# Performance work log

Measured on AMD Instinct MI355X. Metric: run time of the kernel, lower is better.

The kernel has to match this reference:

```python
import jax, jax.numpy as jnp
import numpy as np

D_MODEL = 1024
NUM_HEADS = 16
D_HEAD = D_MODEL // NUM_HEADS
MAX_LEN = 16384
BATCH = 4
SEQ = 1024


def setup_inputs() -> dict:
    key = jax.random.key(0)
    ks = jax.random.split(key, 10)
    s = 1.0 / np.sqrt(D_MODEL)
    return {
        "q_in": jax.random.normal(ks[0], (BATCH, SEQ, D_MODEL), jnp.float32),
        "k_in": jax.random.normal(ks[1], (BATCH, SEQ, D_MODEL), jnp.float32),
        "v_in": jax.random.normal(ks[2], (BATCH, SEQ, D_MODEL), jnp.float32),
        "Wq": jax.random.normal(ks[3], (D_MODEL, D_MODEL), jnp.float32) * s,
        "bq": jnp.zeros((D_MODEL,), jnp.float32),
        "Wk": jax.random.normal(ks[4], (D_MODEL, D_MODEL), jnp.float32) * s,
        "bk": jnp.zeros((D_MODEL,), jnp.float32),
        "Wv": jax.random.normal(ks[5], (D_MODEL, D_MODEL), jnp.float32) * s,
        "bv": jnp.zeros((D_MODEL,), jnp.float32),
        "Er": jax.random.normal(ks[6], (MAX_LEN, D_HEAD), jnp.float32),
    }


def _skew(QEr):
    # QEr: [B, H, S, S] -> pad one zero column on the left, reshape, drop row 0
    B, H, S, _ = QEr.shape
    padded = jnp.pad(QEr, ((0, 0), (0, 0), (0, 0), (1, 0)))  # [B,H,S,S+1]
    reshaped = padded.reshape(B, H, S + 1, S)
    return reshaped[:, :, 1:, :]  # [B,H,S,S]


def reference(q_in, k_in, v_in, Wq, bq, Wk, bk, Wv, bv, Er):
    B, S, _ = q_in.shape
    H, Dh = NUM_HEADS, D_HEAD
    # projections, split into heads: [B, H, S, Dh]
    q = (q_in @ Wq + bq).reshape(B, S, H, Dh).transpose(0, 2, 1, 3)
    k = (k_in @ Wk + bk).reshape(B, S, H, Dh).transpose(0, 2, 1, 3)
    v = (v_in @ Wv + bv).reshape(B, S, H, Dh).transpose(0, 2, 1, 3)
    # relative position scores: Er slice [S, Dh]
    Er_sl = Er[MAX_LEN - S:, :]
    QEr = jnp.einsum('bhsd,td->bhst', q, Er_sl)  # [B,H,S,S]
    Srel = _skew(QEr)
    QK = jnp.einsum('bhsd,bhtd->bhst', q, k)
    attn = (QK + Srel) / jnp.sqrt(jnp.asarray(Dh, q.dtype))
    attn = jax.nn.softmax(attn, axis=-1)
    out = jnp.einsum('bhst,bhtd->bhsd', attn, v)  # [B,H,S,Dh]
    out = out.transpose(0, 2, 1, 3).reshape(B, S, H * Dh)
    return out
```

## Files before the change

kernel.cpp:

```cpp
#include <hip/hip_runtime.h>
#include <hip/hip_bf16.h>
#include <cstdint>

#define S_LEN 1024
#define DMODEL 1024
#define NHEADS 16
#define DHEAD 64
#define MAXLEN 16384
#define BATCH 4

typedef __attribute__((ext_vector_type(8))) short bf16x8;
typedef __attribute__((ext_vector_type(4))) float f32x4;

#define AS1(p) ((const __attribute__((address_space(1))) unsigned int*)(p))
#define AS3(p) ((__attribute__((address_space(3))) unsigned int*)(p))

__device__ inline unsigned short f2b(float f) {
  unsigned int u = __float_as_uint(f);
  unsigned int r = (u + 0x7FFFu + ((u >> 16) & 1u)) >> 16;
  return (unsigned short)r;
}
__device__ inline float b2f(unsigned short u) {
  return __uint_as_float(((unsigned int)u) << 16);
}

#define LDSWZ(row, slot) (((row) << 6) + (((slot) ^ ((row) & 7)) << 3))

__global__ __launch_bounds__(256) void wt_er_convert(
    const float* __restrict__ W0, const float* __restrict__ W1, const float* __restrict__ W2,
    unsigned short* __restrict__ T0, unsigned short* __restrict__ T1, unsigned short* __restrict__ T2,
    const float* __restrict__ Er, unsigned short* __restrict__ Erb) {
  const int z = blockIdx.z;
  if (z == 3) {
    const int o = blockIdx.y * 32 + blockIdx.x;
    if (o < 64) {
      const int i = o * 1024 + threadIdx.x * 4;
      float4 f = *(const float4*)(Er + (size_t)(MAXLEN - S_LEN) * DHEAD + i);
      Erb[i] = f2b(f.x); Erb[i + 1] = f2b(f.y);
      Erb[i + 2] = f2b(f.z); Erb[i + 3] = f2b(f.w);
    }
    return;
  }
  const float* W = (z == 0) ? W0 : (z == 1) ? W1 : W2;
  unsigned short* WT = (z == 0) ? T0 : (z == 1) ? T1 : T2;
  __shared__ float t[32][33];
  const int bi = blockIdx.y * 32, bj = blockIdx.x * 32;
  const int r = threadIdx.x >> 3, c4 = (threadIdx.x & 7) * 4;
  float4 f = *(const float4*)&W[(size_t)(bi + r) * DMODEL + bj + c4];
  t[r][c4] = f.x; t[r][c4 + 1] = f.y; t[r][c4 + 2] = f.z; t[r][c4 + 3] = f.w;
  __syncthreads();
  ushort4 u;
  u.x = f2b(t[c4][r]); u.y = f2b(t[c4 + 1][r]);
  u.z = f2b(t[c4 + 2][r]); u.w = f2b(t[c4 + 3][r]);
  *(ushort4*)&WT[(size_t)(bj + r) * DMODEL + bi + c4] = u;
}

__global__ __launch_bounds__(256) void xconvert3(
    const float* __restrict__ X0, const float* __restrict__ X1, const float* __restrict__ X2,
    unsigned short* __restrict__ B0, unsigned short* __restrict__ B1, unsigned short* __restrict__ B2) {
  const int z = blockIdx.z;
  const float* X = (z == 0) ? X0 : (z == 1) ? X1 : X2;
  unsigned short* B = (z == 0) ? B0 : (z == 1) ? B1 : B2;
  size_t i = ((size_t)blockIdx.x * 256 + threadIdx.x) * 16;
  union { unsigned short h[16]; int4 v[2]; } u;
#pragma unroll
  for (int r = 0; r < 4; ++r) {
    float4 f = *(const float4*)(X + i + r * 4);
    u.h[r * 4 + 0] = f2b(f.x); u.h[r * 4 + 1] = f2b(f.y);
    u.h[r * 4 + 2] = f2b(f.z); u.h[r * 4 + 3] = f2b(f.w);
  }
  *(int4*)(B + i) = u.v[0];
  *(int4*)(B + i + 8) = u.v[1];
}

__global__ __launch_bounds__(256) void proj_glds3(
    const unsigned short* __restrict__ Xq, const unsigned short* __restrict__ Xk,
    const unsigned short* __restrict__ Xv,
    const unsigned short* __restrict__ T0, const unsigned short* __restrict__ T1,
    const unsigned short* __restrict__ T2,
    const float* __restrict__ b0, const float* __restrict__ b1, const float* __restrict__ b2,
    unsigned short* __restrict__ O0, unsigned short* __restrict__ O1,
    unsigned short* __restrict__ O2) {
  const int z = blockIdx.z;
  const unsigned short* X = (z == 0) ? Xq : (z == 1) ? Xk : Xv;
  const unsigned short* WT = (z == 0) ? T0 : (z == 1) ? T1 : T2;
  const float* bias = (z == 0) ? b0 : (z == 1) ? b1 : b2;
  unsigned short* Out = (z == 0) ? O0 : (z == 1) ? O1 : O2;
  const float osc = (z == 0) ? 0.125f : 1.0f;
  __shared__ unsigned short As[128 * 64];
  __shared__ unsigned short Bs[128 * 64];
  const int tid = threadIdx.x;
  const int l = tid & 63, w = tid >> 6;
  const int o = blockIdx.y * 8 + blockIdx.x;
  const int lid = (o & 7) * 32 + (o >> 3);
  const int bm = (lid >> 3) * 128, bn = (lid & 7) * 128;
  const int wr = (w >> 1) * 64, wc = (w & 1) * 64;
  const int lrow = l >> 3;
  const int slotlog = (l & 7) ^ (lrow & 7);
  const unsigned short* Xa = X + (size_t)(bm + lrow) * DMODEL + slotlog * 8;
  const unsigned short* Wa = WT + (size_t)(bn + lrow) * DMODEL + slotlog * 8;
  f32x4 acc[4][4] = {};
  for (int k0 = 0; k0 < DMODEL; k0 += 64) {
    __syncthreads();
#pragma unroll
    for (int j = 0; j < 4; ++j) {
      int r8 = (w * 4 + j) * 8;
      __builtin_amdgcn_global_load_lds(AS1(Xa + (size_t)r8 * DMODEL + k0),
                                       AS3(&As[(w * 4 + j) * 512]), 16, 0, 0);
      __builtin_amdgcn_global_load_lds(AS1(Wa + (size_t)r8 * DMODEL + k0),
                                       AS3(&Bs[(w * 4 + j) * 512]), 16, 0, 0);
    }
    __syncthreads();
#pragma unroll
    for (int ks = 0; ks < 2; ++ks) {
      bf16x8 a[4], b[4];
#pragma unroll
      for (int f = 0; f < 4; ++f) {
        int row = wr + f * 16 + (l & 15);
        a[f] = *(const bf16x8*)&As[LDSWZ(row, ks * 4 + (l >> 4))];
        int col = wc + f * 16 + (l & 15);
        b[f] = *(const bf16x8*)&Bs[LDSWZ(col, ks * 4 + (l >> 4))];
      }
#pragma unroll
      for (int i = 0; i < 4; ++i)
#pragma unroll
        for (int j = 0; j < 4; ++j)
          acc[i][j] = __builtin_amdgcn_mfma_f32_16x16x32_bf16(a[i], b[j], acc[i][j], 0, 0, 0);
    }
  }
#pragma unroll
  for (int i = 0; i < 4; ++i) {
    int m = bm + wr + i * 16 + ((l >> 4) << 2);
#pragma unroll
    for (int j = 0; j < 4; ++j) {
      int n = bn + wc + j * 16 + (l & 15);
      float bv = bias[n];
#pragma unroll
      for (int e = 0; e < 4; ++e)
        Out[(size_t)(m + e) * DMODEL + n] = f2b((acc[i][j][e] + bv) * osc);
    }
  }
}

__global__ __launch_bounds__(256) void qer_mfma(const unsigned short* __restrict__ qp,
    const unsigned short* __restrict__ Erb, unsigned short* __restrict__ G, int bh0) {
  const int bh = bh0 + blockIdx.z;
  const int b = bh >> 4, h = bh & 15;
  __shared__ unsigned short As[128 * 64];
  __shared__ unsigned short Bs[128 * 64];
  const int tid = threadIdx.x, l = tid & 63, wid = tid >> 6;
  const int bm = blockIdx.y * 128, bn = blockIdx.x * 128;
  const int wr = (wid >> 1) * 64, wc = (wid & 1) * 64;
  const unsigned short* qb = qp + (size_t)b * S_LEN * DMODEL + h * DHEAD;
  unsigned short* Gc = G + (size_t)blockIdx.z * S_LEN * S_LEN;
#pragma unroll
  for (int r = 0; r < 4; ++r) {
    int s = r * 256 + tid;
    int row = s >> 3, sl = s & 7;
    *(int4*)&As[LDSWZ(row, sl)] = *(const int4*)(qb + (size_t)(bm + row) * DMODEL + sl * 8);
    *(int4*)&Bs[LDSWZ(row, sl)] = *(const int4*)(Erb + (size_t)(bn + row) * DHEAD + sl * 8);
  }
  if (blockIdx.x == 0 && tid < 128) {
    int s = bm + tid;
    if (s < S_LEN - 1) Gc[(size_t)s * S_LEN + s + 1] = 0;
  }
  __syncthreads();
  f32x4 acc[4][4] = {};
#pragma unroll
  for (int ks = 0; ks < 2; ++ks) {
    bf16x8 a[4], b[4];
#pragma unroll
    for (int f = 0; f < 4; ++f) {
      int row = wr + f * 16 + (l & 15);
      a[f] = *(const bf16x8*)&As[LDSWZ(row, ks * 4 + (l >> 4))];
      int col = wc + f * 16 + (l & 15);
      b[f] = *(const bf16x8*)&Bs[LDSWZ(col, ks * 4 + (l >> 4))];
    }
#pragma unroll
    for (int i = 0; i < 4; ++i)
#pragma unroll
      for (int j = 0; j < 4; ++j)
        acc[i][j] = __builtin_amdgcn_mfma_f32_16x16x32_bf16(a[i], b[j], acc[i][j], 0, 0, 0);
  }
#pragma unroll
  for (int i = 0; i < 4; ++i) {
    int m = bm + wr + i * 16 + ((l >> 4) << 2);
#pragma unroll
    for (int j = 0; j < 4; ++j) {
      int n = bn + wc + j * 16 + (l & 15);
#pragma unroll
      for (int e = 0; e < 4; ++e) {
        int s = m + e;
        int hi = (n >= 1023 - s);
        int r_ = hi ? s : s - 1;
        int t_ = hi ? (n + s - 1023) : (n + s + 1);
        if (r_ >= 0)
          Gc[(size_t)r_ * S_LEN + t_] = f2b(acc[i][j][e]);
      }
    }
  }
}

__global__ __launch_bounds__(256) void attn_skew(const unsigned short* __restrict__ qp,
    const unsigned short* __restrict__ kp, const unsigned short* __restrict__ vp,
    const unsigned short* __restrict__ G, float* __restrict__ out, int bh0) {
  const int bh = bh0 + blockIdx.y;
  const int b = bh >> 4, h = bh & 15;
  const int s0 = blockIdx.x * 64;
  __shared__ unsigned short Qs[64 * 64];
  __shared__ unsigned short Ks[64 * 64];
  __shared__ unsigned short Vt[64 * 64];
  __shared__ unsigned short Ps[4][16 * 64];
  const int tid = threadIdx.x, l = tid & 63, w = tid >> 6;
  const int lg = l >> 4, li = l & 15;
  const unsigned short* qb = qp + (size_t)b * S_LEN * DMODEL + h * DHEAD;
  const unsigned short* kb = kp + (size_t)b * S_LEN * DMODEL + h * DHEAD;
  const unsigned short* vb = vp + (size_t)b * S_LEN * DMODEL + h * DHEAD;
  const unsigned short* Gb = G + (size_t)blockIdx.y * S_LEN * S_LEN;

#pragma unroll
  for (int r = 0; r < 2; ++r) {
    int s = r * 256 + tid;
    int row = s >> 3, sl = s & 7;
    *(int4*)&Qs[LDSWZ(row, sl)] = *(const int4*)(qb + (size_t)(s0 + row) * DMODEL + sl * 8);
  }
  __syncthreads();
  bf16x8 qf[2];
#pragma unroll
  for (int ks = 0; ks < 2; ++ks)
    qf[ks] = *(const bf16x8*)&Qs[LDSWZ(w * 16 + li, ks * 4 + lg)];

  const int lrow = l >> 3;
  const int chk = (l & 7) ^ lrow;
  const unsigned short* Ka = kb + (size_t)(w * 8 + lrow) * DMODEL + chk * 8;

  f32x4 o4[4] = {};
  float lsum[4] = {0.f, 0.f, 0.f, 0.f};
  int sg[4];
  const unsigned short* gp[4];
#pragma unroll
  for (int i = 0; i < 4; ++i) {
    sg[i] = s0 + w * 16 + (lg << 2) + i;
    gp[i] = Gb + (size_t)sg[i] * S_LEN + li;
  }
  const int pr = tid & 31, dh0 = (tid >> 5) * 8;
  const float L2E = 1.44269504f;
  const float SHF = 16.f * 1.44269504f;

  for (int ti = 0; ti < 16; ++ti) {
    const int t0 = ti * 64;
    __syncthreads();
    __builtin_amdgcn_global_load_lds(AS1(Ka + (size_t)t0 * DMODEL),
                                     AS3(&Ks[(w * 64) * 8]), 16, 0, 0);
    __builtin_amdgcn_global_load_lds(AS1(Ka + (size_t)(t0 + 32) * DMODEL),
                                     AS3(&Ks[(256 + w * 64) * 8]), 16, 0, 0);
    {
      const unsigned short* v0p = vb + (size_t)(t0 + pr * 2) * DMODEL + dh0;
      union { int4 v; unsigned short hh[8]; } va, vc;
      va.v = *(const int4*)v0p;
      vc.v = *(const int4*)(v0p + DMODEL);
      unsigned int* vtw = (unsigned int*)Vt;
#pragma unroll
      for (int j = 0; j < 8; ++j) {
        int dh = dh0 + j;
        int widx = dh * 32 + (((pr >> 2) ^ (dh & 7)) << 2) + (pr & 3);
        vtw[widx] = (unsigned int)va.hh[j] | ((unsigned int)vc.hh[j] << 16);
      }
    }
    __syncthreads();
    unsigned short rv[4][4];
#pragma unroll
    for (int f = 0; f < 4; ++f)
#pragma unroll
      for (int i = 0; i < 4; ++i)
        rv[f][i] = gp[i][t0 + f * 16];
    f32x4 sa[4] = {};
#pragma unroll
    for (int ks = 0; ks < 2; ++ks)
#pragma unroll
      for (int f = 0; f < 4; ++f) {
        bf16x8 kf = *(const bf16x8*)&Ks[LDSWZ(f * 16 + li, ks * 4 + lg)];
        sa[f] = __builtin_amdgcn_mfma_f32_16x16x32_bf16(qf[ks], kf, sa[f], 0, 0, 0);
      }
    unsigned short* Pw = &Ps[w][0];
#pragma unroll
    for (int f = 0; f < 4; ++f) {
#pragma unroll
      for (int i = 0; i < 4; ++i) {
        float sv = sa[f][i] + b2f(rv[f][i]);
        float pv = __builtin_exp2f(__builtin_fmaf(sv, L2E, -SHF));
        unsigned int pu = __float_as_uint(pv) & 0xffff0000u;
        lsum[i] += __uint_as_float(pu);
        int prow = (lg << 2) + i, pcol = f * 16 + li;
        Pw[LDSWZ(prow, pcol >> 3) + (pcol & 7)] = (unsigned short)(pu >> 16);
      }
    }
#pragma unroll
    for (int ks = 0; ks < 2; ++ks) {
      bf16x8 pf = *(const bf16x8*)&Pw[LDSWZ(li, ks * 4 + lg)];
#pragma unroll
      for (int f = 0; f < 4; ++f) {
        bf16x8 vf = *(const bf16x8*)&Vt[LDSWZ(f * 16 + li, ks * 4 + lg)];
        o4[f] = __builtin_amdgcn_mfma_f32_16x16x32_bf16(pf, vf, o4[f], 0, 0, 0);
      }
    }
  }
#pragma unroll
  for (int off = 8; off >= 1; off >>= 1)
#pragma unroll
    for (int i = 0; i < 4; ++i) lsum[i] += __shfl_xor(lsum[i], off);
#pragma unroll
  for (int i = 0; i < 4; ++i) {
    float inv = 1.f / lsum[i];
#pragma unroll
    for (int f = 0; f < 4; ++f)
      out[(size_t)(b * S_LEN + sg[i]) * DMODEL + h * DHEAD + f * 16 + li] = o4[f][i] * inv;
  }
}

extern "C" void kernel_launch(void* const* d_in, const int* in_sizes, int n_in,
                              void* d_out, int out_size, void* d_ws, size_t ws_size,
                              hipStream_t stream) {
  (void)in_sizes; (void)n_in; (void)out_size;
  const float* q_in = (const float*)d_in[0];
  const float* k_in = (const float*)d_in[1];
  const float* v_in = (const float*)d_in[2];
  const float* Wq   = (const float*)d_in[3];
  const float* bq   = (const float*)d_in[4];
  const float* Wk   = (const float*)d_in[5];
  const float* bk   = (const float*)d_in[6];
  const float* Wv   = (const float*)d_in[7];
  const float* bv   = (const float*)d_in[8];
  const float* Er   = (const float*)d_in[9];
  float* out = (float*)d_out;

  char* ws = (char*)d_ws;
  const size_t MB = (size_t)1 << 20;
  unsigned short* wtq = (unsigned short*)(ws);
  unsigned short* wtk = (unsigned short*)(ws + 2 * MB);
  unsigned short* wtv = (unsigned short*)(ws + 4 * MB);
  unsigned short* erb = (unsigned short*)(ws + 6 * MB);
  unsigned short* qp  = (unsigned short*)(ws + 8 * MB);
  unsigned short* kp  = (unsigned short*)(ws + 16 * MB);
  unsigned short* vp  = (unsigned short*)(ws + 24 * MB);
  unsigned short* xq  = (unsigned short*)(ws + 32 * MB);
  unsigned short* xk  = (unsigned short*)(ws + 40 * MB);
  unsigned short* xv  = (unsigned short*)(ws + 48 * MB);
  unsigned short* G   = (unsigned short*)(ws + 56 * MB);

  const size_t gavail = (ws_size > 56 * MB) ? (ws_size - 56 * MB) : 0;
  int chunk = (int)(gavail / (2 * MB));
  if (chunk < 1) chunk = 1;
  if (chunk > 64) chunk = 64;

  dim3 blk(256);
  hipLaunchKernelGGL(wt_er_convert, dim3(32, 32, 4), blk, 0, stream,
                     Wq, Wk, Wv, wtq, wtk, wtv, Er, erb);
  hipLaunchKernelGGL(xconvert3, dim3(1024, 1, 3), blk, 0, stream,
                     q_in, k_in, v_in, xq, xk, xv);

  dim3 gproj(DMODEL / 128, (BATCH * S_LEN) / 128, 3);
  hipLaunchKernelGGL(proj_glds3, gproj, blk, 0, stream,
                     xq, xk, xv, wtq, wtk, wtv, bq, bk, bv, qp, kp, vp);

  for (int bh0 = 0; bh0 < BATCH * NHEADS; bh0 += chunk) {
    int nb = BATCH * NHEADS - bh0;
    if (nb > chunk) nb = chunk;
    dim3 gqer(S_LEN / 128, S_LEN / 128, nb);
    hipLaunchKernelGGL(qer_mfma, gqer, blk, 0, stream, qp, erb, G, bh0);
    dim3 gattn(S_LEN / 64, nb);
    hipLaunchKernelGGL(attn_skew, gattn, blk, 0, stream, qp, kp, vp, G, out, bh0);
  }
}
```

Baseline: 161.8 us.

## Merge convert kernels, prefetch skew tile, remap attention blocks, seed MFMA accumulator

Folds the weight/Er and activation fp32-to-bf16 conversions into a single launch to save one kernel launch. In the attention kernel, the next tile's skewed relative-position values are prefetched into registers (double-buffered A/B) while the current tile computes, hiding global load latency. The relative term is now used as the initial MFMA accumulator instead of being added afterwards. Block indices are also remapped so consecutive blocks go to different heads, which may change L2 and XCD locality; the cost is higher register pressure and an unrolled body.

```diff
diff --git a/kernel.cpp b/kernel.cpp
--- a/kernel.cpp
+++ b/kernel.cpp
@@ -26,11 +26,28 @@
 
 #define LDSWZ(row, slot) (((row) << 6) + (((slot) ^ ((row) & 7)) << 3))
 
-__global__ __launch_bounds__(256) void wt_er_convert(
+__global__ __launch_bounds__(256) void convert_all(
     const float* __restrict__ W0, const float* __restrict__ W1, const float* __restrict__ W2,
     unsigned short* __restrict__ T0, unsigned short* __restrict__ T1, unsigned short* __restrict__ T2,
-    const float* __restrict__ Er, unsigned short* __restrict__ Erb) {
+    const float* __restrict__ Er, unsigned short* __restrict__ Erb,
+    const float* __restrict__ X0, const float* __restrict__ X1, const float* __restrict__ X2,
+    unsigned short* __restrict__ B0, unsigned short* __restrict__ B1, unsigned short* __restrict__ B2) {
   const int z = blockIdx.z;
+  if (z >= 4) {
+    const float* X = (z == 4) ? X0 : (z == 5) ? X1 : X2;
+    unsigned short* B = (z == 4) ? B0 : (z == 5) ? B1 : B2;
+    size_t i = (((size_t)blockIdx.y * 32 + blockIdx.x) * 256 + threadIdx.x) * 16;
+    union { unsigned short hh[16]; int4 v[2]; } u;
+#pragma unroll
+    for (int r = 0; r < 4; ++r) {
+      float4 f = *(const float4*)(X + i + r * 4);
+      u.hh[r * 4 + 0] = f2b(f.x); u.hh[r * 4 + 1] = f2b(f.y);
+      u.hh[r * 4 + 2] = f2b(f.z); u.hh[r * 4 + 3] = f2b(f.w);
+    }
+    *(int4*)(B + i) = u.v[0];
+    *(int4*)(B + i + 8) = u.v[1];
+    return;
+  }
   if (z == 3) {
     const int o = blockIdx.y * 32 + blockIdx.x;
     if (o < 64) {
@@ -53,24 +70,6 @@
   u.x = f2b(t[c4][r]); u.y = f2b(t[c4 + 1][r]);
   u.z = f2b(t[c4 + 2][r]); u.w = f2b(t[c4 + 3][r]);
   *(ushort4*)&WT[(size_t)(bj + r) * DMODEL + bi + c4] = u;
-}
-
-__global__ __launch_bounds__(256) void xconvert3(
-    const float* __restrict__ X0, const float* __restrict__ X1, const float* __restrict__ X2,
-    unsigned short* __restrict__ B0, unsigned short* __restrict__ B1, unsigned short* __restrict__ B2) {
-  const int z = blockIdx.z;
-  const float* X = (z == 0) ? X0 : (z == 1) ? X1 : X2;
-  unsigned short* B = (z == 0) ? B0 : (z == 1) ? B1 : B2;
-  size_t i = ((size_t)blockIdx.x * 256 + threadIdx.x) * 16;
-  union { unsigned short h[16]; int4 v[2]; } u;
-#pragma unroll
-  for (int r = 0; r < 4; ++r) {
-    float4 f = *(const float4*)(X + i + r * 4);
-    u.h[r * 4 + 0] = f2b(f.x); u.h[r * 4 + 1] = f2b(f.y);
-    u.h[r * 4 + 2] = f2b(f.z); u.h[r * 4 + 3] = f2b(f.w);
-  }
-  *(int4*)(B + i) = u.v[0];
-  *(int4*)(B + i + 8) = u.v[1];
 }
 
 __global__ __launch_bounds__(256) void proj_glds3(
@@ -203,10 +202,14 @@
 
 __global__ __launch_bounds__(256) void attn_skew(const unsigned short* __restrict__ qp,
     const unsigned short* __restrict__ kp, const unsigned short* __restrict__ vp,
-    const unsigned short* __restrict__ G, float* __restrict__ out, int bh0) {
-  const int bh = bh0 + blockIdx.y;
+    const unsigned short* __restrict__ G, float* __restrict__ out, int bh0, int nb) {
+  const int o = blockIdx.y * 16 + blockIdx.x;
+  const int q8 = nb * 2;
+  const int lid = (o & 7) * q8 + (o >> 3);
+  const int s0 = (lid & 15) * 64;
+  const int bhl = lid >> 4;
+  const int bh = bh0 + bhl;
   const int b = bh >> 4, h = bh & 15;
-  const int s0 = blockIdx.x * 64;
   __shared__ unsigned short Qs[64 * 64];
   __shared__ unsigned short Ks[64 * 64];
   __shared__ unsigned short Vt[64 * 64];
@@ -216,7 +219,7 @@
   const unsigned short* qb = qp + (size_t)b * S_LEN * DMODEL + h * DHEAD;
   const unsigned short* kb = kp + (size_t)b * S_LEN * DMODEL + h * DHEAD;
   const unsigned short* vb = vp + (size_t)b * S_LEN * DMODEL + h * DHEAD;
-  const unsigned short* Gb = G + (size_t)blockIdx.y * S_LEN * S_LEN;
+  const unsigned short* Gb = G + (size_t)bhl * S_LEN * S_LEN;
 
 #pragma unroll
   for (int r = 0; r < 2; ++r) {
@@ -224,6 +227,18 @@
     int row = s >> 3, sl = s & 7;
     *(int4*)&Qs[LDSWZ(row, sl)] = *(const int4*)(qb + (size_t)(s0 + row) * DMODEL + sl * 8);
   }
+  int sg[4];
+  const unsigned short* gp[4];
+#pragma unroll
+  for (int i = 0; i < 4; ++i) {
+    sg[i] = s0 + w * 16 + (lg << 2) + i;
+    gp[i] = Gb + (size_t)sg[i] * S_LEN + li;
+  }
+  unsigned short rvA[4][4], rvB[4][4];
+#pragma unroll
+  for (int f = 0; f < 4; ++f)
+#pragma unroll
+    for (int i = 0; i < 4; ++i) rvA[f][i] = gp[i][f * 16];
   __syncthreads();
   bf16x8 qf[2];
 #pragma unroll
@@ -236,75 +251,84 @@
 
   f32x4 o4[4] = {};
   float lsum[4] = {0.f, 0.f, 0.f, 0.f};
-  int sg[4];
-  const unsigned short* gp[4];
-#pragma unroll
-  for (int i = 0; i < 4; ++i) {
-    sg[i] = s0 + w * 16 + (lg << 2) + i;
-    gp[i] = Gb + (size_t)sg[i] * S_LEN + li;
-  }
   const int pr = tid & 31, dh0 = (tid >> 5) * 8;
   const float L2E = 1.44269504f;
   const float SHF = 16.f * 1.44269504f;
 
-  for (int ti = 0; ti < 16; ++ti) {
-    const int t0 = ti * 64;
-    __syncthreads();
-    __builtin_amdgcn_global_load_lds(AS1(Ka + (size_t)t0 * DMODEL),
-                                     AS3(&Ks[(w * 64) * 8]), 16, 0, 0);
-    __builtin_amdgcn_global_load_lds(AS1(Ka + (size_t)(t0 + 32) * DMODEL),
-                                     AS3(&Ks[(256 + w * 64) * 8]), 16, 0, 0);
-    {
-      const unsigned short* v0p = vb + (size_t)(t0 + pr * 2) * DMODEL + dh0;
-      union { int4 v; unsigned short hh[8]; } va, vc;
-      va.v = *(const int4*)v0p;
-      vc.v = *(const int4*)(v0p + DMODEL);
-      unsigned int* vtw = (unsigned int*)Vt;
-#pragma unroll
-      for (int j = 0; j < 8; ++j) {
-        int dh = dh0 + j;
-        int widx = dh * 32 + (((pr >> 2) ^ (dh & 7)) << 2) + (pr & 3);
-        vtw[widx] = (unsigned int)va.hh[j] | ((unsigned int)vc.hh[j] << 16);
-      }
-    }
-    __syncthreads();
-    unsigned short rv[4][4];
-#pragma unroll
-    for (int f = 0; f < 4; ++f)
-#pragma unroll
-      for (int i = 0; i < 4; ++i)
-        rv[f][i] = gp[i][t0 + f * 16];
-    f32x4 sa[4] = {};
-#pragma unroll
-    for (int ks = 0; ks < 2; ++ks)
-#pragma unroll
-      for (int f = 0; f < 4; ++f) {
-        bf16x8 kf = *(const bf16x8*)&Ks[LDSWZ(f * 16 + li, ks * 4 + lg)];
-        sa[f] = __builtin_amdgcn_mfma_f32_16x16x32_bf16(qf[ks], kf, sa[f], 0, 0, 0);
-      }
-    unsigned short* Pw = &Ps[w][0];
-#pragma unroll
-    for (int f = 0; f < 4; ++f) {
-#pragma unroll
-      for (int i = 0; i < 4; ++i) {
-        float sv = sa[f][i] + b2f(rv[f][i]);
-        float pv = __builtin_exp2f(__builtin_fmaf(sv, L2E, -SHF));
-        unsigned int pu = __float_as_uint(pv) & 0xffff0000u;
-        lsum[i] += __uint_as_float(pu);
-        int prow = (lg << 2) + i, pcol = f * 16 + li;
-        Pw[LDSWZ(prow, pcol >> 3) + (pcol & 7)] = (unsigned short)(pu >> 16);
-      }
-    }
-#pragma unroll
-    for (int ks = 0; ks < 2; ++ks) {
-      bf16x8 pf = *(const bf16x8*)&Pw[LDSWZ(li, ks * 4 + lg)];
-#pragma unroll
-      for (int f = 0; f < 4; ++f) {
-        bf16x8 vf = *(const bf16x8*)&Vt[LDSWZ(f * 16 + li, ks * 4 + lg)];
-        o4[f] = __builtin_amdgcn_mfma_f32_16x16x32_bf16(pf, vf, o4[f], 0, 0, 0);
-      }
-    }
-  }
+#define ATTN_BODY(TI, RC, RN)                                                  \
+  {                                                                            \
+    const int t0 = (TI) * 64;                                                  \
+    __syncthreads();                       \
+    __builtin_amdgcn_global_load_lds(AS1(Ka + (size_t)t0 * DMODEL),            \
+                                     AS3(&Ks[(w * 64) * 8]), 16, 0, 0);        \
+    __builtin_amdgcn_global_load_lds(AS1(Ka + (size_t)(t0 + 32) * DMODEL),     \
+                                     AS3(&Ks[(256 + w * 64) * 8]), 16, 0, 0);  \
+    {                      \
+      const unsigned short* v0p = vb + (size_t)(t0 + pr * 2) * DMODEL + dh0;   \
+      union { int4 v; unsigned short hh[8]; } va, vc;                          \
+      va.v = *(const int4*)v0p;                                                \
+      vc.v = *(const int4*)(v0p + DMODEL);                                     \
+      unsigned int* vtw = (unsigned int*)Vt;                                   \
+      _Pragma("unroll")                                                        \
+      for (int j = 0; j < 8; ++j) {                                            \
+        int dh = dh0 + j;                                                      \
+        int widx = dh * 32 + (((pr >> 2) ^ (dh & 7)) << 2) + (pr & 3);         \
+        vtw[widx] = (unsigned int)va.hh[j] | ((unsigned int)vc.hh[j] << 16);   \
+      }                                                                        \
+    }                                                                          \
+    __syncthreads();                          \
+                    \
+    f32x4 sa[4];                                                               \
+    _Pragma("unroll")                                                          \
+    for (int f = 0; f < 4; ++f) {                                              \
+      sa[f][0] = b2f(RC[f][0]); sa[f][1] = b2f(RC[f][1]);                      \
+      sa[f][2] = b2f(RC[f][2]); sa[f][3] = b2f(RC[f][3]);                      \
+    }                                                                          \
+    _Pragma("unroll")                                                          \
+    for (int ks = 0; ks < 2; ++ks)                                             \
+      _Pragma("unroll")                                                        \
+      for (int f = 0; f < 4; ++f) {                                            \
+        bf16x8 kf = *(const bf16x8*)&Ks[LDSWZ(f * 16 + li, ks * 4 + lg)];      \
+        sa[f] = __builtin_amdgcn_mfma_f32_16x16x32_bf16(qf[ks], kf, sa[f],     \
+                                                        0, 0, 0);              \
+      }                                                                        \
+    if ((TI) < 15) {    \
+      _Pragma("unroll")                                                        \
+      for (int f = 0; f < 4; ++f)                                              \
+        _Pragma("unroll")                                                      \
+        for (int i = 0; i < 4; ++i) RN[f][i] = gp[i][t0 + 64 + f * 16];        \
+    }                                                                          \
+              \
+    unsigned short* Pw = &Ps[w][0];                                            \
+    _Pragma("unroll")                                                          \
+    for (int f = 0; f < 4; ++f) {                                              \
+      _Pragma("unroll")                                                        \
+      for (int i = 0; i < 4; ++i) {                                            \
+        float pv = __builtin_exp2f(__builtin_fmaf(sa[f][i], L2E, -SHF));       \
+        unsigned int pu = __float_as_uint(pv) & 0xffff0000u;                   \
+        lsum[i] += __uint_as_float(pu);                                        \
+        int prow = (lg << 2) + i, pcol = f * 16 + li;                          \
+        Pw[LDSWZ(prow, pcol >> 3) + (pcol & 7)] = (unsigned short)(pu >> 16);  \
+      }                                                                        \
+    }                                                                          \
+    _Pragma("unroll")                                                          \
+    for (int ks = 0; ks < 2; ++ks) {                                           \
+      bf16x8 pf = *(const bf16x8*)&Pw[LDSWZ(li, ks * 4 + lg)];                 \
+      _Pragma("unroll")                                                        \
+      for (int f = 0; f < 4; ++f) {                                            \
+        bf16x8 vf = *(const bf16x8*)&Vt[LDSWZ(f * 16 + li, ks * 4 + lg)];      \
+        o4[f] = __builtin_amdgcn_mfma_f32_16x16x32_bf16(pf, vf, o4[f],         \
+                                                        0, 0, 0);              \
+      }                                                                        \
+    }                                                                          \
+  }
+
+  for (int tt = 0; tt < 8; ++tt) {
+    ATTN_BODY(tt * 2, rvA, rvB);
+    ATTN_BODY(tt * 2 + 1, rvB, rvA);
+  }
+#undef ATTN_BODY
+
 #pragma unroll
   for (int off = 8; off >= 1; off >>= 1)
 #pragma unroll
@@ -354,9 +378,8 @@
   if (chunk > 64) chunk = 64;
 
   dim3 blk(256);
-  hipLaunchKernelGGL(wt_er_convert, dim3(32, 32, 4), blk, 0, stream,
-                     Wq, Wk, Wv, wtq, wtk, wtv, Er, erb);
-  hipLaunchKernelGGL(xconvert3, dim3(1024, 1, 3), blk, 0, stream,
+  hipLaunchKernelGGL(convert_all, dim3(32, 32, 7), blk, 0, stream,
+                     Wq, Wk, Wv, wtq, wtk, wtv, Er, erb,
                      q_in, k_in, v_in, xq, xk, xv);
 
   dim3 gproj(DMODEL / 128, (BATCH * S_LEN) / 128, 3);
@@ -368,7 +391,7 @@
     if (nb > chunk) nb = chunk;
     dim3 gqer(S_LEN / 128, S_LEN / 128, nb);
     hipLaunchKernelGGL(qer_mfma, gqer, blk, 0, stream, qp, erb, G, bh0);
-    dim3 gattn(S_LEN / 64, nb);
-    hipLaunchKernelGGL(attn_skew, gattn, blk, 0, stream, qp, kp, vp, G, out, bh0);
-  }
-}
+    dim3 gattn(16, nb);
+    hipLaunchKernelGGL(attn_skew, gattn, blk, 0, stream, qp, kp, vp, G, out, bh0, nb);
+  }
+}
```

Result: slower. 166.4 us (+2.9%).
